# Optimization experiments

Hardware: AMD Instinct MI355X
Metric: run time of the kernel (lower is better)

Reference implementation:

```python
import jax, jax.numpy as jnp
import numpy as np

N = 100000
E = 1600000
IN, HID, OUT = 128, 64, 32


def setup_inputs() -> dict:
    key = jax.random.key(0)
    k1, k2, k3, k4, k5, k6 = jax.random.split(key, 6)
    x = jax.random.normal(k1, (N, IN), dtype=jnp.float32)
    edge_index = jax.random.randint(k2, (2, E), 0, N, dtype=jnp.int64)
    # Glorot-style init for the two GCNConv layers (weight + bias each)
    W1 = jax.random.normal(k3, (IN, HID), dtype=jnp.float32) / np.sqrt(IN)
    b1 = jnp.zeros((HID,), dtype=jnp.float32)
    W2 = jax.random.normal(k4, (HID, OUT), dtype=jnp.float32) / np.sqrt(HID)
    b2 = jnp.zeros((OUT,), dtype=jnp.float32)
    return {"x": x, "edge_index": edge_index, "W1": W1, "b1": b1, "W2": W2, "b2": b2}


def _gcn_norm(edge_index, n, dtype):
    """Add self-loops and compute symmetric normalization coefficients.
    Returns (row, col, norm) where norm[e] = deg[row]^-1/2 * deg[col]^-1/2."""
    loops = jnp.tile(jnp.arange(n, dtype=edge_index.dtype)[None, :], (2, 1))
    ei = jnp.concatenate([edge_index, loops], axis=1)  # [2, E+N]
    row, col = ei[0], ei[1]
    deg = jax.ops.segment_sum(jnp.ones(col.shape, dtype), col, num_segments=n)
    dinv = jnp.where(deg > 0, jax.lax.rsqrt(deg), 0.0)
    norm = dinv[row] * dinv[col]
    return row, col, norm


def _gcn_conv(h, W, b, row, col, norm, n):
    h = h @ W                                   # [N, F_out] dense transform first
    msg = h[row] * norm[:, None]                # gather + edge-normalize
    out = jax.ops.segment_sum(msg, col, num_segments=n)  # scatter-add
    return out + b


def reference(x, edge_index, W1, b1, W2, b2):
    n = x.shape[0]
    row, col, norm = _gcn_norm(edge_index, n, x.dtype)
    h = jax.nn.relu(_gcn_conv(x, W1, b1, row, col, norm, n))
    return _gcn_conv(h, W2, b2, row, col, norm, n)
```

## Files before the change

kernel.cpp:

```cpp
#include <hip/hip_runtime.h>
#include <hip/hip_fp16.h>


#define CDIV(a, b) (((a) + (b)-1) / (b))
#define EDGE_TILE 8192
#define BUCKET_CAP 4608

__device__ inline unsigned short f2h(float f) {
    __half h = __float2half_rn(f);
    return __half_as_ushort(h);
}
__device__ inline void h2x2(unsigned int u, float& lo, float& hi) {
    __half2 h = *reinterpret_cast<__half2*>(&u);
    lo = __low2float(h);
    hi = __high2float(h);
}

__global__ __launch_bounds__(256, 3) void k_sort_gemm1(
    const int* __restrict__ row, const int* __restrict__ col, int e,
    int* __restrict__ gcur, int* __restrict__ bucket,
    const float* __restrict__ x, const float* __restrict__ W,
    unsigned short* __restrict__ hb, int n, int nb_sort) {
    __shared__ float4 smem4[2560];
    int t = threadIdx.x;
    if ((int)blockIdx.x < nb_sort) {
        int* ints   = (int*)smem4;
        int* hist   = ints;
        int* lstart = ints + 512;
        int* rbase  = ints + 1024;
        int* lcur   = ints + 1536;
        int* ent    = ints + 2048;
        int base = blockIdx.x * EDGE_TILE;
        int cnt = min(EDGE_TILE, e - base);
        int nbuck = (n + 255) >> 8;
        hist[t] = 0; hist[t + 256] = 0;
        __syncthreads();
        for (int i = t; i < cnt; i += 256) atomicAdd(&hist[col[base + i] >> 8], 1);
        __syncthreads();
        int h0 = hist[2 * t], h1 = hist[2 * t + 1];
        int sum2 = h0 + h1;
        lcur[t] = sum2;
        __syncthreads();
        for (int d = 1; d < 256; d <<= 1) {
            int v = (t >= d) ? lcur[t - d] : 0;
            __syncthreads();
            lcur[t] += v;
            __syncthreads();
        }
        int excl2 = lcur[t] - sum2;
        lstart[2 * t] = excl2;
        lstart[2 * t + 1] = excl2 + h0;
        __syncthreads();
        for (int b = t; b < 512; b += 256) {
            int hbv = hist[b];
            rbase[b] = (hbv > 0) ? atomicAdd(&gcur[b], hbv) : 0;
            lcur[b] = 0;
        }
        __syncthreads();
        for (int i = t; i < cnt; i += 256) {
            int c = col[base + i], r = row[base + i];
            int b = c >> 8;
            int rk = atomicAdd(&lcur[b], 1);
            ent[lstart[b] + rk] = ((c & 255) << 17) | r;
        }
        __syncthreads();
        for (int i = t; i < cnt; i += 256) {
            int lo = 0, hi = nbuck - 1;
            while (lo < hi) {
                int mid = (lo + hi + 1) >> 1;
                if (lstart[mid] <= i) lo = mid; else hi = mid - 1;
            }
            int b = lo;
            int gi = rbase[b] + (i - lstart[b]);
            if (gi < BUCKET_CAP) bucket[(size_t)b * BUCKET_CAP + gi] = ent[i];
        }
    } else {
        float4* xs = smem4;
        int base = ((int)blockIdx.x - nb_sort) * 64;
        int nodes = min(64, n - base);
        const float4* xg = (const float4*)(x + (size_t)base * 128);
        int lim = nodes * 32;
#pragma unroll
        for (int i = 0; i < 8; ++i) {
            int idx = t + i * 256;
            if (idx < lim) xs[idx] = xg[idx];
        }
        __syncthreads();
        int j = t & 63, g = t >> 6;
        float acc[16];
#pragma unroll
        for (int mm = 0; mm < 16; ++mm) acc[mm] = 0.f;
#pragma unroll 8
        for (int k4 = 0; k4 < 32; ++k4) {
            float w0 = W[(k4 * 4 + 0) * 64 + j];
            float w1 = W[(k4 * 4 + 1) * 64 + j];
            float w2 = W[(k4 * 4 + 2) * 64 + j];
            float w3 = W[(k4 * 4 + 3) * 64 + j];
#pragma unroll
            for (int mm = 0; mm < 16; ++mm) {
                float4 xv = xs[(mm * 4 + g) * 32 + k4];
                acc[mm] = fmaf(xv.x, w0, acc[mm]);
                acc[mm] = fmaf(xv.y, w1, acc[mm]);
                acc[mm] = fmaf(xv.z, w2, acc[mm]);
                acc[mm] = fmaf(xv.w, w3, acc[mm]);
            }
        }
#pragma unroll
        for (int mm = 0; mm < 16; ++mm) {
            int m = base + mm * 4 + g;
            if (m < n) hb[(size_t)m * 64 + j] = f2h(acc[mm]);
        }
    }
}

__global__ __launch_bounds__(256) void k_csr(
    const int* __restrict__ gcur, const int* __restrict__ bucket,
    int* __restrict__ csr, int* __restrict__ start, int* __restrict__ cntg,
    float* __restrict__ dinv, int n) {
    __shared__ int hist[256], lstart[256], lcur[256], sc[256];
    __shared__ int csrbuf[BUCKET_CAP];
    int b = blockIdx.x, t = threadIdx.x;
    int nb = gridDim.x;
    int* gball = csrbuf;
    int v0 = (2 * t < nb) ? min(gcur[2 * t], BUCKET_CAP) : 0;
    int v1 = (2 * t + 1 < nb) ? min(gcur[2 * t + 1], BUCKET_CAP) : 0;
    int s2 = v0 + v1;
    sc[t] = s2;
    __syncthreads();
    for (int d = 1; d < 256; d <<= 1) {
        int a = (t >= d) ? sc[t - d] : 0;
        __syncthreads();
        sc[t] += a;
        __syncthreads();
    }
    int excl2 = sc[t] - s2;
    gball[2 * t] = excl2;
    gball[2 * t + 1] = excl2 + v0;
    __syncthreads();
    int gb = gball[b];
    int nodebase = b << 8;
    int nnode = min(256, n - nodebase);
    int m = min(gcur[b], BUCKET_CAP);
    const int* ent = bucket + (size_t)b * BUCKET_CAP;
    __syncthreads();
    hist[t] = 0;
    __syncthreads();
    for (int i = t; i < m; i += 256) atomicAdd(&hist[ent[i] >> 17], 1);
    __syncthreads();
    int v = hist[t];
    lstart[t] = v;
    __syncthreads();
    for (int d = 1; d < 256; d <<= 1) {
        int a = (t >= d) ? lstart[t - d] : 0;
        __syncthreads();
        lstart[t] += a;
        __syncthreads();
    }
    int excl = lstart[t] - v;
    if (t < nnode) {
        int node = nodebase + t;
        start[node] = gb + excl;
        cntg[node] = v;
        dinv[node] = rsqrtf((float)(v + 1));
    }
    __syncthreads();
    lstart[t] = excl;
    lcur[t] = 0;
    __syncthreads();
    for (int i = t; i < m; i += 256) {
        int en = ent[i];
        int local = en >> 17;
        int rk = atomicAdd(&lcur[local], 1);
        csrbuf[lstart[local] + rk] = en & 0x1FFFF;
    }
    __syncthreads();
    for (int i = t; i < m; i += 256) csr[gb + i] = csrbuf[i];
}

__global__ __launch_bounds__(256) void k_agg1(const int* __restrict__ start,
                                              const int* __restrict__ cnt,
                                              const int* __restrict__ csr,
                                              const float* __restrict__ dinv,
                                              const unsigned short* __restrict__ hbm,
                                              const float* __restrict__ b,
                                              const float* __restrict__ W2,
                                              unsigned short* __restrict__ h2b, int n) {
    __shared__ float rowbuf[4][64];
    int node = (blockIdx.x * 256 + threadIdx.x) >> 6;
    int w = threadIdx.x >> 6;
    int lane = threadIdx.x & 63;
    int q = lane >> 3;
    int f4 = lane & 7;
    const int* cs = csr + start[node];
    int d = cnt[node];
    float dc = dinv[node];
    const uint4* hb = (const uint4*)hbm;
    float a0[8], a1[8];
#pragma unroll
    for (int k = 0; k < 8; ++k) { a0[k] = 0.f; a1[k] = 0.f; }
    int j = q;
    for (; j + 8 < d; j += 16) {
        int r0 = cs[j], r1 = cs[j + 8];
        float d0 = dinv[r0], d1 = dinv[r1];
        uint4 v0 = hb[(size_t)r0 * 8 + f4];
        uint4 v1 = hb[(size_t)r1 * 8 + f4];
        float lo, hi;
        h2x2(v0.x, lo, hi); a0[0] = fmaf(lo, d0, a0[0]); a0[1] = fmaf(hi, d0, a0[1]);
        h2x2(v0.y, lo, hi); a0[2] = fmaf(lo, d0, a0[2]); a0[3] = fmaf(hi, d0, a0[3]);
        h2x2(v0.z, lo, hi); a0[4] = fmaf(lo, d0, a0[4]); a0[5] = fmaf(hi, d0, a0[5]);
        h2x2(v0.w, lo, hi); a0[6] = fmaf(lo, d0, a0[6]); a0[7] = fmaf(hi, d0, a0[7]);
        h2x2(v1.x, lo, hi); a1[0] = fmaf(lo, d1, a1[0]); a1[1] = fmaf(hi, d1, a1[1]);
        h2x2(v1.y, lo, hi); a1[2] = fmaf(lo, d1, a1[2]); a1[3] = fmaf(hi, d1, a1[3]);
        h2x2(v1.z, lo, hi); a1[4] = fmaf(lo, d1, a1[4]); a1[5] = fmaf(hi, d1, a1[5]);
        h2x2(v1.w, lo, hi); a1[6] = fmaf(lo, d1, a1[6]); a1[7] = fmaf(hi, d1, a1[7]);
    }
    if (j < d) {
        int r = cs[j];
        float d0 = dinv[r];
        uint4 v0 = hb[(size_t)r * 8 + f4];
        float lo, hi;
        h2x2(v0.x, lo, hi); a0[0] = fmaf(lo, d0, a0[0]); a0[1] = fmaf(hi, d0, a0[1]);
        h2x2(v0.y, lo, hi); a0[2] = fmaf(lo, d0, a0[2]); a0[3] = fmaf(hi, d0, a0[3]);
        h2x2(v0.z, lo, hi); a0[4] = fmaf(lo, d0, a0[4]); a0[5] = fmaf(hi, d0, a0[5]);
        h2x2(v0.w, lo, hi); a0[6] = fmaf(lo, d0, a0[6]); a0[7] = fmaf(hi, d0, a0[7]);
    }
#pragma unroll
    for (int k = 0; k < 8; ++k) a0[k] += a1[k];
#pragma unroll
    for (int k = 0; k < 8; ++k) {
        a0[k] += __shfl_xor(a0[k], 8, 64);
        a0[k] += __shfl_xor(a0[k], 16, 64);
        a0[k] += __shfl_xor(a0[k], 32, 64);
    }
    if (q == 0) {
        uint4 sv = hb[(size_t)node * 8 + f4];
        float s[8], lo, hi;
        h2x2(sv.x, lo, hi); s[0] = lo; s[1] = hi;
        h2x2(sv.y, lo, hi); s[2] = lo; s[3] = hi;
        h2x2(sv.z, lo, hi); s[4] = lo; s[5] = hi;
        h2x2(sv.w, lo, hi); s[6] = lo; s[7] = hi;
        const float4* b4 = (const float4*)b;
        float4 bv0 = b4[f4 * 2], bv1 = b4[f4 * 2 + 1];
        rowbuf[w][f4 * 8 + 0] = fmaxf(fmaf(s[0], dc, a0[0]) * dc + bv0.x, 0.f);
        rowbuf[w][f4 * 8 + 1] = fmaxf(fmaf(s[1], dc, a0[1]) * dc + bv0.y, 0.f);
        rowbuf[w][f4 * 8 + 2] = fmaxf(fmaf(s[2], dc, a0[2]) * dc + bv0.z, 0.f);
        rowbuf[w][f4 * 8 + 3] = fmaxf(fmaf(s[3], dc, a0[3]) * dc + bv0.w, 0.f);
        rowbuf[w][f4 * 8 + 4] = fmaxf(fmaf(s[4], dc, a0[4]) * dc + bv1.x, 0.f);
        rowbuf[w][f4 * 8 + 5] = fmaxf(fmaf(s[5], dc, a0[5]) * dc + bv1.y, 0.f);
        rowbuf[w][f4 * 8 + 6] = fmaxf(fmaf(s[6], dc, a0[6]) * dc + bv1.z, 0.f);
        rowbuf[w][f4 * 8 + 7] = fmaxf(fmaf(s[7], dc, a0[7]) * dc + bv1.w, 0.f);
    }
    __syncthreads();
    int jj = lane & 31, half = lane >> 5;
    const float* rw = rowbuf[w] + half * 32;
    const float* Wk = W2 + half * 32 * 32 + jj;
    float acc = 0.f;
#pragma unroll 8
    for (int k = 0; k < 32; ++k) acc = fmaf(rw[k], Wk[k * 32], acc);
    acc += __shfl_xor(acc, 32, 64);
    if (half == 0) h2b[(size_t)node * 32 + jj] = f2h(acc * dc);
}

__global__ __launch_bounds__(256) void k_agg2(const int* __restrict__ start,
                                              const int* __restrict__ cnt,
                                              const int* __restrict__ csr,
                                              const float* __restrict__ dinv,
                                              const unsigned short* __restrict__ hbm,
                                              const float* __restrict__ b,
                                              float* __restrict__ out, int n) {
    int node = (blockIdx.x * 256 + threadIdx.x) >> 6;
    if (node >= n) return;
    int lane = threadIdx.x & 63;
    int q = lane >> 2;
    int f4 = lane & 3;
    const int* cs = csr + start[node];
    int d = cnt[node];
    const uint4* hb = (const uint4*)hbm;
    float a0[8], a1[8];
#pragma unroll
    for (int k = 0; k < 8; ++k) { a0[k] = 0.f; a1[k] = 0.f; }
    int j = q;
    for (; j + 16 < d; j += 32) {
        int r0 = cs[j], r1 = cs[j + 16];
        uint4 v0 = hb[(size_t)r0 * 4 + f4];
        uint4 v1 = hb[(size_t)r1 * 4 + f4];
        float lo, hi;
        h2x2(v0.x, lo, hi); a0[0] += lo; a0[1] += hi;
        h2x2(v0.y, lo, hi); a0[2] += lo; a0[3] += hi;
        h2x2(v0.z, lo, hi); a0[4] += lo; a0[5] += hi;
        h2x2(v0.w, lo, hi); a0[6] += lo; a0[7] += hi;
        h2x2(v1.x, lo, hi); a1[0] += lo; a1[1] += hi;
        h2x2(v1.y, lo, hi); a1[2] += lo; a1[3] += hi;
        h2x2(v1.z, lo, hi); a1[4] += lo; a1[5] += hi;
        h2x2(v1.w, lo, hi); a1[6] += lo; a1[7] += hi;
    }
    if (j < d) {
        int r = cs[j];
        uint4 v0 = hb[(size_t)r * 4 + f4];
        float lo, hi;
        h2x2(v0.x, lo, hi); a0[0] += lo; a0[1] += hi;
        h2x2(v0.y, lo, hi); a0[2] += lo; a0[3] += hi;
        h2x2(v0.z, lo, hi); a0[4] += lo; a0[5] += hi;
        h2x2(v0.w, lo, hi); a0[6] += lo; a0[7] += hi;
    }
#pragma unroll
    for (int k = 0; k < 8; ++k) a0[k] += a1[k];
#pragma unroll
    for (int k = 0; k < 8; ++k) {
        a0[k] += __shfl_xor(a0[k], 4, 64);
        a0[k] += __shfl_xor(a0[k], 8, 64);
        a0[k] += __shfl_xor(a0[k], 16, 64);
        a0[k] += __shfl_xor(a0[k], 32, 64);
    }
    if (q == 0) {
        float dc = dinv[node];
        uint4 sv = hb[(size_t)node * 4 + f4];
        float s[8], lo, hi;
        h2x2(sv.x, lo, hi); s[0] = lo; s[1] = hi;
        h2x2(sv.y, lo, hi); s[2] = lo; s[3] = hi;
        h2x2(sv.z, lo, hi); s[4] = lo; s[5] = hi;
        h2x2(sv.w, lo, hi); s[6] = lo; s[7] = hi;
        const float4* b4 = (const float4*)b;
        float4 bv0 = b4[f4 * 2], bv1 = b4[f4 * 2 + 1];
        float4 o0, o1;
        o0.x = (a0[0] + s[0]) * dc + bv0.x;
        o0.y = (a0[1] + s[1]) * dc + bv0.y;
        o0.z = (a0[2] + s[2]) * dc + bv0.z;
        o0.w = (a0[3] + s[3]) * dc + bv0.w;
        o1.x = (a0[4] + s[4]) * dc + bv1.x;
        o1.y = (a0[5] + s[5]) * dc + bv1.y;
        o1.z = (a0[6] + s[6]) * dc + bv1.z;
        o1.w = (a0[7] + s[7]) * dc + bv1.w;
        float4* o4 = (float4*)out;
        o4[(size_t)node * 8 + f4 * 2]     = o0;
        o4[(size_t)node * 8 + f4 * 2 + 1] = o1;
    }
}

extern "C" void kernel_launch(void* const* d_in, const int* in_sizes, int n_in,
                              void* d_out, int out_size, void* d_ws, size_t ws_size,
                              hipStream_t stream) {
    const float* x  = (const float*)d_in[0];
    const int*   ei = (const int*)d_in[1];
    const float* W1 = (const float*)d_in[2];
    const float* b1 = (const float*)d_in[3];
    const float* W2 = (const float*)d_in[4];
    const float* b2 = (const float*)d_in[5];
    float* out = (float*)d_out;

    const int n = in_sizes[0] / 128;
    const int e = in_sizes[1] / 2;
    const int* rowp = ei;
    const int* colp = ei + e;

    const int nbuck = CDIV(n, 256);
    const int nb_sort = CDIV(e, EDGE_TILE);
    const int nb_gemm1 = CDIV(n, 64);

    int*   gcur  = (int*)d_ws;
    int*   start = gcur + 512;
    int*   cnt   = start + n;
    float* dinv  = (float*)(cnt + n);
    int*   csr   = (int*)(dinv + n);
    unsigned short* h1h = (unsigned short*)(csr + e);
    int*   bucket = (int*)(h1h + (size_t)n * 64);
    unsigned short* h2h = (unsigned short*)bucket;

    hipMemsetAsync(gcur, 0, 512 * sizeof(int), stream);

    k_sort_gemm1<<<nb_sort + nb_gemm1, 256, 0, stream>>>(
        rowp, colp, e, gcur, bucket, x, W1, h1h, n, nb_sort);
    k_csr<<<nbuck, 256, 0, stream>>>(gcur, bucket, csr, start, cnt, dinv, n);

    k_agg1<<<CDIV(n * 64, 256), 256, 0, stream>>>(start, cnt, csr, dinv, h1h, b1, W2, h2h, n);
    k_agg2<<<CDIV(n * 64, 256), 256, 0, stream>>>(start, cnt, csr, dinv, h2h, b2, out, n);
}
```

Baseline: 261.9 us.

## Map one wavefront per node with lane-per-feature gathers in aggregation kernels

```diff
diff --git a/kernel.cpp b/kernel.cpp
--- a/kernel.cpp
+++ b/kernel.cpp
@@ -9,11 +9,6 @@
 __device__ inline unsigned short f2h(float f) {
     __half h = __float2half_rn(f);
     return __half_as_ushort(h);
-}
-__device__ inline void h2x2(unsigned int u, float& lo, float& hi) {
-    __half2 h = *reinterpret_cast<__half2*>(&u);
-    lo = __low2float(h);
-    hi = __high2float(h);
 }
 
 __global__ __launch_bounds__(256, 3) void k_sort_gemm1(
@@ -86,29 +81,36 @@
             if (idx < lim) xs[idx] = xg[idx];
         }
         __syncthreads();
-        int j = t & 63, g = t >> 6;
-        float acc[16];
-#pragma unroll
-        for (int mm = 0; mm < 16; ++mm) acc[mm] = 0.f;
+        int j = t & 31, g = t >> 5;
+        float acc0[8], acc1[8];
+#pragma unroll
+        for (int mm = 0; mm < 8; ++mm) { acc0[mm] = 0.f; acc1[mm] = 0.f; }
 #pragma unroll 8
         for (int k4 = 0; k4 < 32; ++k4) {
-            float w0 = W[(k4 * 4 + 0) * 64 + j];
-            float w1 = W[(k4 * 4 + 1) * 64 + j];
-            float w2 = W[(k4 * 4 + 2) * 64 + j];
-            float w3 = W[(k4 * 4 + 3) * 64 + j];
-#pragma unroll
-            for (int mm = 0; mm < 16; ++mm) {
-                float4 xv = xs[(mm * 4 + g) * 32 + k4];
-                acc[mm] = fmaf(xv.x, w0, acc[mm]);
-                acc[mm] = fmaf(xv.y, w1, acc[mm]);
-                acc[mm] = fmaf(xv.z, w2, acc[mm]);
-                acc[mm] = fmaf(xv.w, w3, acc[mm]);
+            float w00 = W[(k4 * 4 + 0) * 64 + j], w10 = W[(k4 * 4 + 0) * 64 + j + 32];
+            float w01 = W[(k4 * 4 + 1) * 64 + j], w11 = W[(k4 * 4 + 1) * 64 + j + 32];
+            float w02 = W[(k4 * 4 + 2) * 64 + j], w12 = W[(k4 * 4 + 2) * 64 + j + 32];
+            float w03 = W[(k4 * 4 + 3) * 64 + j], w13 = W[(k4 * 4 + 3) * 64 + j + 32];
+#pragma unroll
+            for (int mm = 0; mm < 8; ++mm) {
+                float4 xv = xs[(mm * 8 + g) * 32 + k4];
+                acc0[mm] = fmaf(xv.x, w00, acc0[mm]);
+                acc0[mm] = fmaf(xv.y, w01, acc0[mm]);
+                acc0[mm] = fmaf(xv.z, w02, acc0[mm]);
+                acc0[mm] = fmaf(xv.w, w03, acc0[mm]);
+                acc1[mm] = fmaf(xv.x, w10, acc1[mm]);
+                acc1[mm] = fmaf(xv.y, w11, acc1[mm]);
+                acc1[mm] = fmaf(xv.z, w12, acc1[mm]);
+                acc1[mm] = fmaf(xv.w, w13, acc1[mm]);
             }
         }
 #pragma unroll
-        for (int mm = 0; mm < 16; ++mm) {
-            int m = base + mm * 4 + g;
-            if (m < n) hb[(size_t)m * 64 + j] = f2h(acc[mm]);
+        for (int mm = 0; mm < 8; ++mm) {
+            int m = base + mm * 8 + g;
+            if (m < n) {
+                hb[(size_t)m * 64 + j]      = f2h(acc0[mm]);
+                hb[(size_t)m * 64 + j + 32] = f2h(acc1[mm]);
+            }
         }
     }
 }
@@ -186,71 +188,39 @@
                                               const float* __restrict__ W2,
                                               unsigned short* __restrict__ h2b, int n) {
     __shared__ float rowbuf[4][64];
-    int node = (blockIdx.x * 256 + threadIdx.x) >> 6;
     int w = threadIdx.x >> 6;
     int lane = threadIdx.x & 63;
-    int q = lane >> 3;
-    int f4 = lane & 7;
+    int node = __builtin_amdgcn_readfirstlane((int)blockIdx.x * 4 + w);
     const int* cs = csr + start[node];
     int d = cnt[node];
     float dc = dinv[node];
-    const uint4* hb = (const uint4*)hbm;
-    float a0[8], a1[8];
-#pragma unroll
-    for (int k = 0; k < 8; ++k) { a0[k] = 0.f; a1[k] = 0.f; }
-    int j = q;
-    for (; j + 8 < d; j += 16) {
-        int r0 = cs[j], r1 = cs[j + 8];
-        float d0 = dinv[r0], d1 = dinv[r1];
-        uint4 v0 = hb[(size_t)r0 * 8 + f4];
-        uint4 v1 = hb[(size_t)r1 * 8 + f4];
-        float lo, hi;
-        h2x2(v0.x, lo, hi); a0[0] = fmaf(lo, d0, a0[0]); a0[1] = fmaf(hi, d0, a0[1]);
-        h2x2(v0.y, lo, hi); a0[2] = fmaf(lo, d0, a0[2]); a0[3] = fmaf(hi, d0, a0[3]);
-        h2x2(v0.z, lo, hi); a0[4] = fmaf(lo, d0, a0[4]); a0[5] = fmaf(hi, d0, a0[5]);
-        h2x2(v0.w, lo, hi); a0[6] = fmaf(lo, d0, a0[6]); a0[7] = fmaf(hi, d0, a0[7]);
-        h2x2(v1.x, lo, hi); a1[0] = fmaf(lo, d1, a1[0]); a1[1] = fmaf(hi, d1, a1[1]);
-        h2x2(v1.y, lo, hi); a1[2] = fmaf(lo, d1, a1[2]); a1[3] = fmaf(hi, d1, a1[3]);
-        h2x2(v1.z, lo, hi); a1[4] = fmaf(lo, d1, a1[4]); a1[5] = fmaf(hi, d1, a1[5]);
-        h2x2(v1.w, lo, hi); a1[6] = fmaf(lo, d1, a1[6]); a1[7] = fmaf(hi, d1, a1[7]);
+    const __half* hp = (const __half*)hbm;
+    float a = 0.f;
+    int j = 0;
+    for (; j + 8 <= d; j += 8) {
+#pragma unroll
+        for (int u = 0; u < 8; ++u) {
+            int r = cs[j + u];
+            float dr = dinv[r];
+            float v = __half2float(hp[(size_t)r * 64 + lane]);
+            a = fmaf(v, dr, a);
+        }
     }
     if (j < d) {
-        int r = cs[j];
-        float d0 = dinv[r];
-        uint4 v0 = hb[(size_t)r * 8 + f4];
-        float lo, hi;
-        h2x2(v0.x, lo, hi); a0[0] = fmaf(lo, d0, a0[0]); a0[1] = fmaf(hi, d0, a0[1]);
-        h2x2(v0.y, lo, hi); a0[2] = fmaf(lo, d0, a0[2]); a0[3] = fmaf(hi, d0, a0[3]);
-        h2x2(v0.z, lo, hi); a0[4] = fmaf(lo, d0, a0[4]); a0[5] = fmaf(hi, d0, a0[5]);
-        h2x2(v0.w, lo, hi); a0[6] = fmaf(lo, d0, a0[6]); a0[7] = fmaf(hi, d0, a0[7]);
-    }
-#pragma unroll
-    for (int k = 0; k < 8; ++k) a0[k] += a1[k];
-#pragma unroll
-    for (int k = 0; k < 8; ++k) {
-        a0[k] += __shfl_xor(a0[k], 8, 64);
-        a0[k] += __shfl_xor(a0[k], 16, 64);
-        a0[k] += __shfl_xor(a0[k], 32, 64);
-    }
-    if (q == 0) {
-        uint4 sv = hb[(size_t)node * 8 + f4];
-        float s[8], lo, hi;
-        h2x2(sv.x, lo, hi); s[0] = lo; s[1] = hi;
-        h2x2(sv.y, lo, hi); s[2] = lo; s[3] = hi;
-        h2x2(sv.z, lo, hi); s[4] = lo; s[5] = hi;
-        h2x2(sv.w, lo, hi); s[6] = lo; s[7] = hi;
-        const float4* b4 = (const float4*)b;
-        float4 bv0 = b4[f4 * 2], bv1 = b4[f4 * 2 + 1];
-        rowbuf[w][f4 * 8 + 0] = fmaxf(fmaf(s[0], dc, a0[0]) * dc + bv0.x, 0.f);
-        rowbuf[w][f4 * 8 + 1] = fmaxf(fmaf(s[1], dc, a0[1]) * dc + bv0.y, 0.f);
-        rowbuf[w][f4 * 8 + 2] = fmaxf(fmaf(s[2], dc, a0[2]) * dc + bv0.z, 0.f);
-        rowbuf[w][f4 * 8 + 3] = fmaxf(fmaf(s[3], dc, a0[3]) * dc + bv0.w, 0.f);
-        rowbuf[w][f4 * 8 + 4] = fmaxf(fmaf(s[4], dc, a0[4]) * dc + bv1.x, 0.f);
-        rowbuf[w][f4 * 8 + 5] = fmaxf(fmaf(s[5], dc, a0[5]) * dc + bv1.y, 0.f);
-        rowbuf[w][f4 * 8 + 6] = fmaxf(fmaf(s[6], dc, a0[6]) * dc + bv1.z, 0.f);
-        rowbuf[w][f4 * 8 + 7] = fmaxf(fmaf(s[7], dc, a0[7]) * dc + bv1.w, 0.f);
-    }
-    __syncthreads();
+#pragma unroll
+        for (int u = 0; u < 8; ++u) {
+            int iu = j + u;
+            int idx = (iu < d) ? iu : 0;
+            int r = cs[idx];
+            float dr = (iu < d) ? dinv[r] : 0.0f;
+            float v = __half2float(hp[(size_t)r * 64 + lane]);
+            a = fmaf(v, dr, a);
+        }
+    }
+    float sv = __half2float(hp[(size_t)node * 64 + lane]);
+    float bv = b[lane];
+    float rv = fmaxf(fmaf(sv, dc, a) * dc + bv, 0.f);
+    rowbuf[w][lane] = rv;
     int jj = lane & 31, half = lane >> 5;
     const float* rw = rowbuf[w] + half * 32;
     const float* Wk = W2 + half * 32 * 32 + jj;
@@ -268,72 +238,45 @@
                                               const unsigned short* __restrict__ hbm,
                                               const float* __restrict__ b,
                                               float* __restrict__ out, int n) {
-    int node = (blockIdx.x * 256 + threadIdx.x) >> 6;
-    if (node >= n) return;
+    int w = threadIdx.x >> 6;
     int lane = threadIdx.x & 63;
-    int q = lane >> 2;
-    int f4 = lane & 3;
+    int node = __builtin_amdgcn_readfirstlane((int)blockIdx.x * 4 + w);
+    int f = lane & 31, half = lane >> 5;
     const int* cs = csr + start[node];
     int d = cnt[node];
-    const uint4* hb = (const uint4*)hbm;
-    float a0[8], a1[8];
-#pragma unroll
-    for (int k = 0; k < 8; ++k) { a0[k] = 0.f; a1[k] = 0.f; }
-    int j = q;
-    for (; j + 16 < d; j += 32) {
-        int r0 = cs[j], r1 = cs[j + 16];
-        uint4 v0 = hb[(size_t)r0 * 4 + f4];
-        uint4 v1 = hb[(size_t)r1 * 4 + f4];
-        float lo, hi;
-        h2x2(v0.x, lo, hi); a0[0] += lo; a0[1] += hi;
-        h2x2(v0.y, lo, hi); a0[2] += lo; a0[3] += hi;
-        h2x2(v0.z, lo, hi); a0[4] += lo; a0[5] += hi;
-        h2x2(v0.w, lo, hi); a0[6] += lo; a0[7] += hi;
-        h2x2(v1.x, lo, hi); a1[0] += lo; a1[1] += hi;
-        h2x2(v1.y, lo, hi); a1[2] += lo; a1[3] += hi;
-        h2x2(v1.z, lo, hi); a1[4] += lo; a1[5] += hi;
-        h2x2(v1.w, lo, hi); a1[6] += lo; a1[7] += hi;
+    float dc = dinv[node];
+    const __half* hp = (const __half*)hbm;
+    float a = 0.f;
+    int j = 0;
+    for (; j + 8 <= d; j += 8) {
+#pragma unroll
+        for (int p = 0; p < 4; ++p) {
+            int r0 = cs[j + 2 * p];
+            int r1 = cs[j + 2 * p + 1];
+            int r = half ? r1 : r0;
+            a += __half2float(hp[(size_t)r * 32 + f]);
+        }
     }
     if (j < d) {
-        int r = cs[j];
-        uint4 v0 = hb[(size_t)r * 4 + f4];
-        float lo, hi;
-        h2x2(v0.x, lo, hi); a0[0] += lo; a0[1] += hi;
-        h2x2(v0.y, lo, hi); a0[2] += lo; a0[3] += hi;
-        h2x2(v0.z, lo, hi); a0[4] += lo; a0[5] += hi;
-        h2x2(v0.w, lo, hi); a0[6] += lo; a0[7] += hi;
-    }
-#pragma unroll
-    for (int k = 0; k < 8; ++k) a0[k] += a1[k];
-#pragma unroll
-    for (int k = 0; k < 8; ++k) {
-        a0[k] += __shfl_xor(a0[k], 4, 64);
-        a0[k] += __shfl_xor(a0[k], 8, 64);
-        a0[k] += __shfl_xor(a0[k], 16, 64);
-        a0[k] += __shfl_xor(a0[k], 32, 64);
-    }
-    if (q == 0) {
-        float dc = dinv[node];
-        uint4 sv = hb[(size_t)node * 4 + f4];
-        float s[8], lo, hi;
-        h2x2(sv.x, lo, hi); s[0] = lo; s[1] = hi;
-        h2x2(sv.y, lo, hi); s[2] = lo; s[3] = hi;
-        h2x2(sv.z, lo, hi); s[4] = lo; s[5] = hi;
-        h2x2(sv.w, lo, hi); s[6] = lo; s[7] = hi;
-        const float4* b4 = (const float4*)b;
-        float4 bv0 = b4[f4 * 2], bv1 = b4[f4 * 2 + 1];
-        float4 o0, o1;
-        o0.x = (a0[0] + s[0]) * dc + bv0.x;
-        o0.y = (a0[1] + s[1]) * dc + bv0.y;
-        o0.z = (a0[2] + s[2]) * dc + bv0.z;
-        o0.w = (a0[3] + s[3]) * dc + bv0.w;
-        o1.x = (a0[4] + s[4]) * dc + bv1.x;
-        o1.y = (a0[5] + s[5]) * dc + bv1.y;
-        o1.z = (a0[6] + s[6]) * dc + bv1.z;
-        o1.w = (a0[7] + s[7]) * dc + bv1.w;
-        float4* o4 = (float4*)out;
-        o4[(size_t)node * 8 + f4 * 2]     = o0;
-        o4[(size_t)node * 8 + f4 * 2 + 1] = o1;
+#pragma unroll
+        for (int p = 0; p < 4; ++p) {
+            int i0 = j + 2 * p;
+            int idx0 = (i0 < d) ? i0 : 0;
+            int idx1 = (i0 + 1 < d) ? (i0 + 1) : 0;
+            int r0 = cs[idx0];
+            int r1 = cs[idx1];
+            int r = half ? r1 : r0;
+            int isel = i0 + half;
+            float mk = (isel < d) ? 1.0f : 0.0f;
+            float v = __half2float(hp[(size_t)r * 32 + f]);
+            a = fmaf(v, mk, a);
+        }
+    }
+    a += __shfl_xor(a, 32, 64);
+    if (half == 0) {
+        float sv = __half2float(hp[(size_t)node * 32 + f]);
+        float o = (a + sv) * dc + b[f];
+        out[(size_t)node * 32 + f] = o;
     }
 }
 
```

After: 267.1 us. No clear change (+2.0%).

## Fuse CSR build into aggregation kernels and prescale GEMM output by dinv

Applied to the files above, without the earlier changes.

```diff
diff --git a/kernel.cpp b/kernel.cpp
--- a/kernel.cpp
+++ b/kernel.cpp
@@ -16,10 +16,26 @@
     hi = __high2float(h);
 }
 
+__global__ __launch_bounds__(256) void k_deg0(const int* __restrict__ col, int e,
+                                              int* __restrict__ degg) {
+    int i4 = (blockIdx.x * 256 + threadIdx.x) * 4;
+    if (i4 + 3 < e) {
+        int4 c = *(const int4*)(col + i4);
+        atomicAdd(&degg[c.x], 1);
+        atomicAdd(&degg[c.y], 1);
+        atomicAdd(&degg[c.z], 1);
+        atomicAdd(&degg[c.w], 1);
+    } else {
+        int lim = min(i4 + 4, e);
+        for (int k = i4; k < lim; ++k) atomicAdd(&degg[col[k]], 1);
+    }
+}
+
 __global__ __launch_bounds__(256, 3) void k_sort_gemm1(
     const int* __restrict__ row, const int* __restrict__ col, int e,
     int* __restrict__ gcur, int* __restrict__ bucket,
     const float* __restrict__ x, const float* __restrict__ W,
+    const int* __restrict__ degg,
     unsigned short* __restrict__ hb, int n, int nb_sort) {
     __shared__ float4 smem4[2560];
     int t = threadIdx.x;
@@ -86,254 +102,265 @@
             if (idx < lim) xs[idx] = xg[idx];
         }
         __syncthreads();
-        int j = t & 63, g = t >> 6;
-        float acc[16];
-#pragma unroll
-        for (int mm = 0; mm < 16; ++mm) acc[mm] = 0.f;
+        int j = t & 31, g = t >> 5;
+        float acc0[8], acc1[8];
+#pragma unroll
+        for (int mm = 0; mm < 8; ++mm) { acc0[mm] = 0.f; acc1[mm] = 0.f; }
 #pragma unroll 8
         for (int k4 = 0; k4 < 32; ++k4) {
-            float w0 = W[(k4 * 4 + 0) * 64 + j];
-            float w1 = W[(k4 * 4 + 1) * 64 + j];
-            float w2 = W[(k4 * 4 + 2) * 64 + j];
-            float w3 = W[(k4 * 4 + 3) * 64 + j];
-#pragma unroll
-            for (int mm = 0; mm < 16; ++mm) {
-                float4 xv = xs[(mm * 4 + g) * 32 + k4];
-                acc[mm] = fmaf(xv.x, w0, acc[mm]);
-                acc[mm] = fmaf(xv.y, w1, acc[mm]);
-                acc[mm] = fmaf(xv.z, w2, acc[mm]);
-                acc[mm] = fmaf(xv.w, w3, acc[mm]);
+            float w00 = W[(k4 * 4 + 0) * 64 + j], w10 = W[(k4 * 4 + 0) * 64 + j + 32];
+            float w01 = W[(k4 * 4 + 1) * 64 + j], w11 = W[(k4 * 4 + 1) * 64 + j + 32];
+            float w02 = W[(k4 * 4 + 2) * 64 + j], w12 = W[(k4 * 4 + 2) * 64 + j + 32];
+            float w03 = W[(k4 * 4 + 3) * 64 + j], w13 = W[(k4 * 4 + 3) * 64 + j + 32];
+#pragma unroll
+            for (int mm = 0; mm < 8; ++mm) {
+                float4 xv = xs[(mm * 8 + g) * 32 + k4];
+                acc0[mm] = fmaf(xv.x, w00, acc0[mm]);
+                acc0[mm] = fmaf(xv.y, w01, acc0[mm]);
+                acc0[mm] = fmaf(xv.z, w02, acc0[mm]);
+                acc0[mm] = fmaf(xv.w, w03, acc0[mm]);
+                acc1[mm] = fmaf(xv.x, w10, acc1[mm]);
+                acc1[mm] = fmaf(xv.y, w11, acc1[mm]);
+                acc1[mm] = fmaf(xv.z, w12, acc1[mm]);
+                acc1[mm] = fmaf(xv.w, w13, acc1[mm]);
             }
         }
 #pragma unroll
-        for (int mm = 0; mm < 16; ++mm) {
-            int m = base + mm * 4 + g;
-            if (m < n) hb[(size_t)m * 64 + j] = f2h(acc[mm]);
-        }
-    }
-}
-
-__global__ __launch_bounds__(256) void k_csr(
+        for (int mm = 0; mm < 8; ++mm) {
+            int m = base + mm * 8 + g;
+            if (m < n) {
+                float dv = rsqrtf((float)(degg[m] + 1));
+                hb[(size_t)m * 64 + j]      = f2h(acc0[mm] * dv);
+                hb[(size_t)m * 64 + j + 32] = f2h(acc1[mm] * dv);
+            }
+        }
+    }
+}
+
+__global__ __launch_bounds__(512, 4) void k_agg1(
     const int* __restrict__ gcur, const int* __restrict__ bucket,
-    int* __restrict__ csr, int* __restrict__ start, int* __restrict__ cntg,
-    float* __restrict__ dinv, int n) {
-    __shared__ int hist[256], lstart[256], lcur[256], sc[256];
+    const unsigned short* __restrict__ h1s,
+    const float* __restrict__ b1, const float* __restrict__ W2,
+    unsigned short* __restrict__ h2b, int n) {
+    __shared__ int hist[256], lstart[256], lcur[256];
+    __shared__ float dinvl[256];
     __shared__ int csrbuf[BUCKET_CAP];
-    int b = blockIdx.x, t = threadIdx.x;
-    int nb = gridDim.x;
-    int* gball = csrbuf;
-    int v0 = (2 * t < nb) ? min(gcur[2 * t], BUCKET_CAP) : 0;
-    int v1 = (2 * t + 1 < nb) ? min(gcur[2 * t + 1], BUCKET_CAP) : 0;
-    int s2 = v0 + v1;
-    sc[t] = s2;
-    __syncthreads();
-    for (int d = 1; d < 256; d <<= 1) {
-        int a = (t >= d) ? sc[t - d] : 0;
-        __syncthreads();
-        sc[t] += a;
-        __syncthreads();
-    }
-    int excl2 = sc[t] - s2;
-    gball[2 * t] = excl2;
-    gball[2 * t + 1] = excl2 + v0;
-    __syncthreads();
-    int gb = gball[b];
-    int nodebase = b << 8;
-    int nnode = min(256, n - nodebase);
-    int m = min(gcur[b], BUCKET_CAP);
-    const int* ent = bucket + (size_t)b * BUCKET_CAP;
-    __syncthreads();
-    hist[t] = 0;
-    __syncthreads();
-    for (int i = t; i < m; i += 256) atomicAdd(&hist[ent[i] >> 17], 1);
-    __syncthreads();
-    int v = hist[t];
-    lstart[t] = v;
-    __syncthreads();
-    for (int d = 1; d < 256; d <<= 1) {
-        int a = (t >= d) ? lstart[t - d] : 0;
-        __syncthreads();
-        lstart[t] += a;
-        __syncthreads();
-    }
-    int excl = lstart[t] - v;
-    if (t < nnode) {
-        int node = nodebase + t;
-        start[node] = gb + excl;
-        cntg[node] = v;
-        dinv[node] = rsqrtf((float)(v + 1));
-    }
-    __syncthreads();
-    lstart[t] = excl;
-    lcur[t] = 0;
-    __syncthreads();
-    for (int i = t; i < m; i += 256) {
+    __shared__ float rowbuf[8][64];
+    int t = threadIdx.x;
+    int bb = blockIdx.x >> 1, hb2 = blockIdx.x & 1;
+    int nodebase = bb << 8;
+    int m = min(gcur[bb], BUCKET_CAP);
+    const int* ent = bucket + (size_t)bb * BUCKET_CAP;
+    if (t < 256) hist[t] = 0;
+    __syncthreads();
+    for (int i = t; i < m; i += 512) atomicAdd(&hist[ent[i] >> 17], 1);
+    __syncthreads();
+    int v = 0, excl = 0;
+    if (t < 256) { v = hist[t]; lstart[t] = v; }
+    __syncthreads();
+    for (int dd = 1; dd < 256; dd <<= 1) {
+        int a = 0;
+        if (t >= dd && t < 256) a = lstart[t - dd];
+        __syncthreads();
+        if (t < 256) lstart[t] += a;
+        __syncthreads();
+    }
+    if (t < 256) {
+        excl = lstart[t] - v;
+        dinvl[t] = rsqrtf((float)(v + 1));
+    }
+    __syncthreads();
+    if (t < 256) { lstart[t] = excl; lcur[t] = 0; }
+    __syncthreads();
+    for (int i = t; i < m; i += 512) {
         int en = ent[i];
         int local = en >> 17;
         int rk = atomicAdd(&lcur[local], 1);
         csrbuf[lstart[local] + rk] = en & 0x1FFFF;
     }
     __syncthreads();
-    for (int i = t; i < m; i += 256) csr[gb + i] = csrbuf[i];
-}
-
-__global__ __launch_bounds__(256) void k_agg1(const int* __restrict__ start,
-                                              const int* __restrict__ cnt,
-                                              const int* __restrict__ csr,
-                                              const float* __restrict__ dinv,
-                                              const unsigned short* __restrict__ hbm,
-                                              const float* __restrict__ b,
-                                              const float* __restrict__ W2,
-                                              unsigned short* __restrict__ h2b, int n) {
-    __shared__ float rowbuf[4][64];
-    int node = (blockIdx.x * 256 + threadIdx.x) >> 6;
-    int w = threadIdx.x >> 6;
-    int lane = threadIdx.x & 63;
-    int q = lane >> 3;
-    int f4 = lane & 7;
-    const int* cs = csr + start[node];
-    int d = cnt[node];
-    float dc = dinv[node];
-    const uint4* hb = (const uint4*)hbm;
-    float a0[8], a1[8];
-#pragma unroll
-    for (int k = 0; k < 8; ++k) { a0[k] = 0.f; a1[k] = 0.f; }
-    int j = q;
-    for (; j + 8 < d; j += 16) {
-        int r0 = cs[j], r1 = cs[j + 8];
-        float d0 = dinv[r0], d1 = dinv[r1];
-        uint4 v0 = hb[(size_t)r0 * 8 + f4];
-        uint4 v1 = hb[(size_t)r1 * 8 + f4];
-        float lo, hi;
-        h2x2(v0.x, lo, hi); a0[0] = fmaf(lo, d0, a0[0]); a0[1] = fmaf(hi, d0, a0[1]);
-        h2x2(v0.y, lo, hi); a0[2] = fmaf(lo, d0, a0[2]); a0[3] = fmaf(hi, d0, a0[3]);
-        h2x2(v0.z, lo, hi); a0[4] = fmaf(lo, d0, a0[4]); a0[5] = fmaf(hi, d0, a0[5]);
-        h2x2(v0.w, lo, hi); a0[6] = fmaf(lo, d0, a0[6]); a0[7] = fmaf(hi, d0, a0[7]);
-        h2x2(v1.x, lo, hi); a1[0] = fmaf(lo, d1, a1[0]); a1[1] = fmaf(hi, d1, a1[1]);
-        h2x2(v1.y, lo, hi); a1[2] = fmaf(lo, d1, a1[2]); a1[3] = fmaf(hi, d1, a1[3]);
-        h2x2(v1.z, lo, hi); a1[4] = fmaf(lo, d1, a1[4]); a1[5] = fmaf(hi, d1, a1[5]);
-        h2x2(v1.w, lo, hi); a1[6] = fmaf(lo, d1, a1[6]); a1[7] = fmaf(hi, d1, a1[7]);
-    }
-    if (j < d) {
-        int r = cs[j];
-        float d0 = dinv[r];
-        uint4 v0 = hb[(size_t)r * 8 + f4];
-        float lo, hi;
-        h2x2(v0.x, lo, hi); a0[0] = fmaf(lo, d0, a0[0]); a0[1] = fmaf(hi, d0, a0[1]);
-        h2x2(v0.y, lo, hi); a0[2] = fmaf(lo, d0, a0[2]); a0[3] = fmaf(hi, d0, a0[3]);
-        h2x2(v0.z, lo, hi); a0[4] = fmaf(lo, d0, a0[4]); a0[5] = fmaf(hi, d0, a0[5]);
-        h2x2(v0.w, lo, hi); a0[6] = fmaf(lo, d0, a0[6]); a0[7] = fmaf(hi, d0, a0[7]);
-    }
-#pragma unroll
-    for (int k = 0; k < 8; ++k) a0[k] += a1[k];
-#pragma unroll
-    for (int k = 0; k < 8; ++k) {
-        a0[k] += __shfl_xor(a0[k], 8, 64);
-        a0[k] += __shfl_xor(a0[k], 16, 64);
-        a0[k] += __shfl_xor(a0[k], 32, 64);
-    }
-    if (q == 0) {
-        uint4 sv = hb[(size_t)node * 8 + f4];
-        float s[8], lo, hi;
-        h2x2(sv.x, lo, hi); s[0] = lo; s[1] = hi;
-        h2x2(sv.y, lo, hi); s[2] = lo; s[3] = hi;
-        h2x2(sv.z, lo, hi); s[4] = lo; s[5] = hi;
-        h2x2(sv.w, lo, hi); s[6] = lo; s[7] = hi;
-        const float4* b4 = (const float4*)b;
-        float4 bv0 = b4[f4 * 2], bv1 = b4[f4 * 2 + 1];
-        rowbuf[w][f4 * 8 + 0] = fmaxf(fmaf(s[0], dc, a0[0]) * dc + bv0.x, 0.f);
-        rowbuf[w][f4 * 8 + 1] = fmaxf(fmaf(s[1], dc, a0[1]) * dc + bv0.y, 0.f);
-        rowbuf[w][f4 * 8 + 2] = fmaxf(fmaf(s[2], dc, a0[2]) * dc + bv0.z, 0.f);
-        rowbuf[w][f4 * 8 + 3] = fmaxf(fmaf(s[3], dc, a0[3]) * dc + bv0.w, 0.f);
-        rowbuf[w][f4 * 8 + 4] = fmaxf(fmaf(s[4], dc, a0[4]) * dc + bv1.x, 0.f);
-        rowbuf[w][f4 * 8 + 5] = fmaxf(fmaf(s[5], dc, a0[5]) * dc + bv1.y, 0.f);
-        rowbuf[w][f4 * 8 + 6] = fmaxf(fmaf(s[6], dc, a0[6]) * dc + bv1.z, 0.f);
-        rowbuf[w][f4 * 8 + 7] = fmaxf(fmaf(s[7], dc, a0[7]) * dc + bv1.w, 0.f);
-    }
-    __syncthreads();
-    int jj = lane & 31, half = lane >> 5;
-    const float* rw = rowbuf[w] + half * 32;
-    const float* Wk = W2 + half * 32 * 32 + jj;
-    float acc = 0.f;
+    int wave = t >> 6, lane = t & 63;
+    int q = lane >> 3, f4 = lane & 7;
+    const uint4* hbv = (const uint4*)h1s;
+    const float4* b4 = (const float4*)b1;
+    float4 bv0 = b4[f4 * 2], bv1 = b4[f4 * 2 + 1];
+    int jj = lane & 31, halfk = lane >> 5;
+    const float* Wk = W2 + halfk * 32 * 32 + jj;
+    int iend = (hb2 << 7) + 128;
+    for (int ii = (hb2 << 7) + wave; ii < iend; ii += 8) {
+        int node = nodebase + ii;
+        if (node >= n) break;
+        int d = hist[ii];
+        int st = lstart[ii];
+        float dc = dinvl[ii];
+        float a0[8], a1[8];
+#pragma unroll
+        for (int k = 0; k < 8; ++k) { a0[k] = 0.f; a1[k] = 0.f; }
+        int j = q;
+        for (; j + 8 < d; j += 16) {
+            int r0 = csrbuf[st + j], r1 = csrbuf[st + j + 8];
+            uint4 v0 = hbv[(size_t)r0 * 8 + f4];
+            uint4 v1 = hbv[(size_t)r1 * 8 + f4];
+            float lo, hi;
+            h2x2(v0.x, lo, hi); a0[0] += lo; a0[1] += hi;
+            h2x2(v0.y, lo, hi); a0[2] += lo; a0[3] += hi;
+            h2x2(v0.z, lo, hi); a0[4] += lo; a0[5] += hi;
+            h2x2(v0.w, lo, hi); a0[6] += lo; a0[7] += hi;
+            h2x2(v1.x, lo, hi); a1[0] += lo; a1[1] += hi;
+            h2x2(v1.y, lo, hi); a1[2] += lo; a1[3] += hi;
+            h2x2(v1.z, lo, hi); a1[4] += lo; a1[5] += hi;
+            h2x2(v1.w, lo, hi); a1[6] += lo; a1[7] += hi;
+        }
+        if (j < d) {
+            int r0 = csrbuf[st + j];
+            uint4 v0 = hbv[(size_t)r0 * 8 + f4];
+            float lo, hi;
+            h2x2(v0.x, lo, hi); a0[0] += lo; a0[1] += hi;
+            h2x2(v0.y, lo, hi); a0[2] += lo; a0[3] += hi;
+            h2x2(v0.z, lo, hi); a0[4] += lo; a0[5] += hi;
+            h2x2(v0.w, lo, hi); a0[6] += lo; a0[7] += hi;
+        }
+#pragma unroll
+        for (int k = 0; k < 8; ++k) a0[k] += a1[k];
+#pragma unroll
+        for (int k = 0; k < 8; ++k) {
+            a0[k] += __shfl_xor(a0[k], 8, 64);
+            a0[k] += __shfl_xor(a0[k], 16, 64);
+            a0[k] += __shfl_xor(a0[k], 32, 64);
+        }
+        if (q == 0) {
+            uint4 sv = hbv[(size_t)node * 8 + f4];
+            float s[8], lo, hi;
+            h2x2(sv.x, lo, hi); s[0] = lo; s[1] = hi;
+            h2x2(sv.y, lo, hi); s[2] = lo; s[3] = hi;
+            h2x2(sv.z, lo, hi); s[4] = lo; s[5] = hi;
+            h2x2(sv.w, lo, hi); s[6] = lo; s[7] = hi;
+            rowbuf[wave][f4 * 8 + 0] = fmaxf((a0[0] + s[0]) * dc + bv0.x, 0.f);
+            rowbuf[wave][f4 * 8 + 1] = fmaxf((a0[1] + s[1]) * dc + bv0.y, 0.f);
+            rowbuf[wave][f4 * 8 + 2] = fmaxf((a0[2] + s[2]) * dc + bv0.z, 0.f);
+            rowbuf[wave][f4 * 8 + 3] = fmaxf((a0[3] + s[3]) * dc + bv0.w, 0.f);
+            rowbuf[wave][f4 * 8 + 4] = fmaxf((a0[4] + s[4]) * dc + bv1.x, 0.f);
+            rowbuf[wave][f4 * 8 + 5] = fmaxf((a0[5] + s[5]) * dc + bv1.y, 0.f);
+            rowbuf[wave][f4 * 8 + 6] = fmaxf((a0[6] + s[6]) * dc + bv1.z, 0.f);
+            rowbuf[wave][f4 * 8 + 7] = fmaxf((a0[7] + s[7]) * dc + bv1.w, 0.f);
+        }
+        const float* rw = rowbuf[wave] + halfk * 32;
+        float acc = 0.f;
 #pragma unroll 8
-    for (int k = 0; k < 32; ++k) acc = fmaf(rw[k], Wk[k * 32], acc);
-    acc += __shfl_xor(acc, 32, 64);
-    if (half == 0) h2b[(size_t)node * 32 + jj] = f2h(acc * dc);
-}
-
-__global__ __launch_bounds__(256) void k_agg2(const int* __restrict__ start,
-                                              const int* __restrict__ cnt,
-                                              const int* __restrict__ csr,
-                                              const float* __restrict__ dinv,
-                                              const unsigned short* __restrict__ hbm,
-                                              const float* __restrict__ b,
-                                              float* __restrict__ out, int n) {
-    int node = (blockIdx.x * 256 + threadIdx.x) >> 6;
-    if (node >= n) return;
-    int lane = threadIdx.x & 63;
-    int q = lane >> 2;
-    int f4 = lane & 3;
-    const int* cs = csr + start[node];
-    int d = cnt[node];
-    const uint4* hb = (const uint4*)hbm;
-    float a0[8], a1[8];
-#pragma unroll
-    for (int k = 0; k < 8; ++k) { a0[k] = 0.f; a1[k] = 0.f; }
-    int j = q;
-    for (; j + 16 < d; j += 32) {
-        int r0 = cs[j], r1 = cs[j + 16];
-        uint4 v0 = hb[(size_t)r0 * 4 + f4];
-        uint4 v1 = hb[(size_t)r1 * 4 + f4];
-        float lo, hi;
-        h2x2(v0.x, lo, hi); a0[0] += lo; a0[1] += hi;
-        h2x2(v0.y, lo, hi); a0[2] += lo; a0[3] += hi;
-        h2x2(v0.z, lo, hi); a0[4] += lo; a0[5] += hi;
-        h2x2(v0.w, lo, hi); a0[6] += lo; a0[7] += hi;
-        h2x2(v1.x, lo, hi); a1[0] += lo; a1[1] += hi;
-        h2x2(v1.y, lo, hi); a1[2] += lo; a1[3] += hi;
-        h2x2(v1.z, lo, hi); a1[4] += lo; a1[5] += hi;
-        h2x2(v1.w, lo, hi); a1[6] += lo; a1[7] += hi;
-    }
-    if (j < d) {
-        int r = cs[j];
-        uint4 v0 = hb[(size_t)r * 4 + f4];
-        float lo, hi;
-        h2x2(v0.x, lo, hi); a0[0] += lo; a0[1] += hi;
-        h2x2(v0.y, lo, hi); a0[2] += lo; a0[3] += hi;
-        h2x2(v0.z, lo, hi); a0[4] += lo; a0[5] += hi;
-        h2x2(v0.w, lo, hi); a0[6] += lo; a0[7] += hi;
-    }
-#pragma unroll
-    for (int k = 0; k < 8; ++k) a0[k] += a1[k];
-#pragma unroll
-    for (int k = 0; k < 8; ++k) {
-        a0[k] += __shfl_xor(a0[k], 4, 64);
-        a0[k] += __shfl_xor(a0[k], 8, 64);
-        a0[k] += __shfl_xor(a0[k], 16, 64);
-        a0[k] += __shfl_xor(a0[k], 32, 64);
-    }
-    if (q == 0) {
-        float dc = dinv[node];
-        uint4 sv = hb[(size_t)node * 4 + f4];
-        float s[8], lo, hi;
-        h2x2(sv.x, lo, hi); s[0] = lo; s[1] = hi;
-        h2x2(sv.y, lo, hi); s[2] = lo; s[3] = hi;
-        h2x2(sv.z, lo, hi); s[4] = lo; s[5] = hi;
-        h2x2(sv.w, lo, hi); s[6] = lo; s[7] = hi;
-        const float4* b4 = (const float4*)b;
-        float4 bv0 = b4[f4 * 2], bv1 = b4[f4 * 2 + 1];
-        float4 o0, o1;
-        o0.x = (a0[0] + s[0]) * dc + bv0.x;
-        o0.y = (a0[1] + s[1]) * dc + bv0.y;
-        o0.z = (a0[2] + s[2]) * dc + bv0.z;
-        o0.w = (a0[3] + s[3]) * dc + bv0.w;
-        o1.x = (a0[4] + s[4]) * dc + bv1.x;
-        o1.y = (a0[5] + s[5]) * dc + bv1.y;
-        o1.z = (a0[6] + s[6]) * dc + bv1.z;
-        o1.w = (a0[7] + s[7]) * dc + bv1.w;
-        float4* o4 = (float4*)out;
-        o4[(size_t)node * 8 + f4 * 2]     = o0;
-        o4[(size_t)node * 8 + f4 * 2 + 1] = o1;
+        for (int k = 0; k < 32; ++k) acc = fmaf(rw[k], Wk[k * 32], acc);
+        acc += __shfl_xor(acc, 32, 64);
+        if (halfk == 0) h2b[(size_t)node * 32 + jj] = f2h(acc * dc);
+    }
+}
+
+__global__ __launch_bounds__(512, 4) void k_agg2(
+    const int* __restrict__ gcur, const int* __restrict__ bucket,
+    const unsigned short* __restrict__ h2s,
+    const float* __restrict__ b2, float* __restrict__ out, int n) {
+    __shared__ int hist[256], lstart[256], lcur[256];
+    __shared__ float dinvl[256];
+    __shared__ int csrbuf[BUCKET_CAP];
+    int t = threadIdx.x;
+    int bb = blockIdx.x >> 1, hb2 = blockIdx.x & 1;
+    int nodebase = bb << 8;
+    int m = min(gcur[bb], BUCKET_CAP);
+    const int* ent = bucket + (size_t)bb * BUCKET_CAP;
+    if (t < 256) hist[t] = 0;
+    __syncthreads();
+    for (int i = t; i < m; i += 512) atomicAdd(&hist[ent[i] >> 17], 1);
+    __syncthreads();
+    int v = 0, excl = 0;
+    if (t < 256) { v = hist[t]; lstart[t] = v; }
+    __syncthreads();
+    for (int dd = 1; dd < 256; dd <<= 1) {
+        int a = 0;
+        if (t >= dd && t < 256) a = lstart[t - dd];
+        __syncthreads();
+        if (t < 256) lstart[t] += a;
+        __syncthreads();
+    }
+    if (t < 256) {
+        excl = lstart[t] - v;
+        dinvl[t] = rsqrtf((float)(v + 1));
+    }
+    __syncthreads();
+    if (t < 256) { lstart[t] = excl; lcur[t] = 0; }
+    __syncthreads();
+    for (int i = t; i < m; i += 512) {
+        int en = ent[i];
+        int local = en >> 17;
+        int rk = atomicAdd(&lcur[local], 1);
+        csrbuf[lstart[local] + rk] = en & 0x1FFFF;
+    }
+    __syncthreads();
+    int wave = t >> 6, lane = t & 63;
+    int q = lane >> 2, f4 = lane & 3;
+    const uint4* hbv = (const uint4*)h2s;
+    const float4* b4 = (const float4*)b2;
+    float4 bv0 = b4[f4 * 2], bv1 = b4[f4 * 2 + 1];
+    int iend = (hb2 << 7) + 128;
+    for (int ii = (hb2 << 7) + wave; ii < iend; ii += 8) {
+        int node = nodebase + ii;
+        if (node >= n) break;
+        int d = hist[ii];
+        int st = lstart[ii];
+        float dc = dinvl[ii];
+        float a0[8], a1[8];
+#pragma unroll
+        for (int k = 0; k < 8; ++k) { a0[k] = 0.f; a1[k] = 0.f; }
+        int j = q;
+        for (; j + 16 < d; j += 32) {
+            int r0 = csrbuf[st + j], r1 = csrbuf[st + j + 16];
+            uint4 v0 = hbv[(size_t)r0 * 4 + f4];
+            uint4 v1 = hbv[(size_t)r1 * 4 + f4];
+            float lo, hi;
+            h2x2(v0.x, lo, hi); a0[0] += lo; a0[1] += hi;
+            h2x2(v0.y, lo, hi); a0[2] += lo; a0[3] += hi;
+            h2x2(v0.z, lo, hi); a0[4] += lo; a0[5] += hi;
+            h2x2(v0.w, lo, hi); a0[6] += lo; a0[7] += hi;
+            h2x2(v1.x, lo, hi); a1[0] += lo; a1[1] += hi;
+            h2x2(v1.y, lo, hi); a1[2] += lo; a1[3] += hi;
+            h2x2(v1.z, lo, hi); a1[4] += lo; a1[5] += hi;
+            h2x2(v1.w, lo, hi); a1[6] += lo; a1[7] += hi;
+        }
+        if (j < d) {
+            int r0 = csrbuf[st + j];
+            uint4 v0 = hbv[(size_t)r0 * 4 + f4];
+            float lo, hi;
+            h2x2(v0.x, lo, hi); a0[0] += lo; a0[1] += hi;
+            h2x2(v0.y, lo, hi); a0[2] += lo; a0[3] += hi;
+            h2x2(v0.z, lo, hi); a0[4] += lo; a0[5] += hi;
+            h2x2(v0.w, lo, hi); a0[6] += lo; a0[7] += hi;
+        }
+#pragma unroll
+        for (int k = 0; k < 8; ++k) a0[k] += a1[k];
+#pragma unroll
+        for (int k = 0; k < 8; ++k) {
+            a0[k] += __shfl_xor(a0[k], 4, 64);
+            a0[k] += __shfl_xor(a0[k], 8, 64);
+            a0[k] += __shfl_xor(a0[k], 16, 64);
+            a0[k] += __shfl_xor(a0[k], 32, 64);
+        }
+        if (q == 0) {
+            uint4 sv = hbv[(size_t)node * 4 + f4];
+            float s[8], lo, hi;
+            h2x2(sv.x, lo, hi); s[0] = lo; s[1] = hi;
+            h2x2(sv.y, lo, hi); s[2] = lo; s[3] = hi;
+            h2x2(sv.z, lo, hi); s[4] = lo; s[5] = hi;
+            h2x2(sv.w, lo, hi); s[6] = lo; s[7] = hi;
+            float4 o0, o1;
+            o0.x = (a0[0] + s[0]) * dc + bv0.x;
+            o0.y = (a0[1] + s[1]) * dc + bv0.y;
+            o0.z = (a0[2] + s[2]) * dc + bv0.z;
+            o0.w = (a0[3] + s[3]) * dc + bv0.w;
+            o1.x = (a0[4] + s[4]) * dc + bv1.x;
+            o1.y = (a0[5] + s[5]) * dc + bv1.y;
+            o1.z = (a0[6] + s[6]) * dc + bv1.z;
+            o1.w = (a0[7] + s[7]) * dc + bv1.w;
+            float4* o4 = (float4*)out;
+            o4[(size_t)node * 8 + f4 * 2]     = o0;
+            o4[(size_t)node * 8 + f4 * 2 + 1] = o1;
+        }
     }
 }
 
@@ -357,21 +384,17 @@
     const int nb_sort = CDIV(e, EDGE_TILE);
     const int nb_gemm1 = CDIV(n, 64);
 
-    int*   gcur  = (int*)d_ws;
-    int*   start = gcur + 512;
-    int*   cnt   = start + n;
-    float* dinv  = (float*)(cnt + n);
-    int*   csr   = (int*)(dinv + n);
-    unsigned short* h1h = (unsigned short*)(csr + e);
-    int*   bucket = (int*)(h1h + (size_t)n * 64);
-    unsigned short* h2h = (unsigned short*)bucket;
-
-    hipMemsetAsync(gcur, 0, 512 * sizeof(int), stream);
-
+    int* gcur = (int*)d_ws;
+    int* degg = gcur + 512;
+    unsigned short* h1s = (unsigned short*)(degg + n);
+    unsigned short* h2s = h1s + (size_t)n * 64;
+    int* bucket = (int*)(h2s + (size_t)n * 32);
+
+    hipMemsetAsync(gcur, 0, (512 + (size_t)n) * sizeof(int), stream);
+
+    k_deg0<<<CDIV(e, 1024), 256, 0, stream>>>(colp, e, degg);
     k_sort_gemm1<<<nb_sort + nb_gemm1, 256, 0, stream>>>(
-        rowp, colp, e, gcur, bucket, x, W1, h1h, n, nb_sort);
-    k_csr<<<nbuck, 256, 0, stream>>>(gcur, bucket, csr, start, cnt, dinv, n);
-
-    k_agg1<<<CDIV(n * 64, 256), 256, 0, stream>>>(start, cnt, csr, dinv, h1h, b1, W2, h2h, n);
-    k_agg2<<<CDIV(n * 64, 256), 256, 0, stream>>>(start, cnt, csr, dinv, h2h, b2, out, n);
-}
+        rowp, colp, e, gcur, bucket, x, W1, degg, h1s, n, nb_sort);
+    k_agg1<<<nbuck * 2, 512, 0, stream>>>(gcur, bucket, h1s, b1, W2, h2s, n);
+    k_agg2<<<nbuck * 2, 512, 0, stream>>>(gcur, bucket, h2s, b2, out, n);
+}
```

Measured after the change: 340.9 us. 1.3x slower.
